# Optimization experiments

Measured on AMD Instinct MI355X. Metric: run time of the kernel, lower is better.

## Reference

```python
import jax, jax.numpy as jnp
import numpy as np

GRID_INTERVAL = 0.3  # grid_interval init arg (used as module-level global in the original source)
EPS = 1e-12
B, G, M, N_ORB, DIM = 16, 4096, 128, 400, 768


def setup_inputs() -> dict:
    key = jax.random.key(0)
    k1, k2, k3, k4, k5 = jax.random.split(key, 5)
    # distances are physical (positive); avoid d=0 so negative powers in the laplace GTO stay finite
    distance_matrices = jax.random.uniform(k1, (B, G, M), jnp.float32, 0.5, 8.0)
    quantum_numbers = jax.random.randint(k2, (B, M), 0, 3).astype(jnp.int32) + 1  # principal q in {1,2,3}
    atomic_orbitals = jax.random.randint(k3, (B, M), 0, N_ORB)
    N_electrons = jax.random.uniform(k4, (B,), jnp.float32, 2.0, 68.0)
    coefficient_table = jax.random.normal(k5, (N_ORB, DIM), jnp.float32)  # nn.Embedding(N_orbitals, dim)
    zeta_table = jnp.ones((N_ORB, 1), jnp.float32)  # nn.Embedding(N_orbitals, 1), init ones
    return dict(distance_matrices=distance_matrices,
                quantum_numbers=quantum_numbers,
                atomic_orbitals=atomic_orbitals,
                N_electrons=N_electrons,
                coefficient_table=coefficient_table,
                zeta_table=zeta_table)


def _gto_bases(d, q, z):
    """GTO and laplace-GTO basis matrices, normalized over the grid axis.
    d: [B,G,M] distances; q: [B,1,M] principal quantum numbers (float); z: [B,1,M] zetas.
    Block-diagonal pad value 1e6 in the original makes off-block entries exactly 0,
    so the per-molecule batched norm over axis=1 matches the block-diagonal column norm.
    """
    e = jnp.exp(-(z ** 2) * d ** 2)
    gto = d ** (q - 1.0) * e  # d^(q-1) * exp(-z^2 d^2)
    denom = jnp.maximum(jnp.linalg.norm(gto, axis=1, keepdims=True), EPS) * GRID_INTERVAL ** 1.5
    l_gto = d ** (q - 3.0) * e * (4.0 * z ** 4 * d ** 4
                                  - 2.0 * z ** 2 * (2.0 * q + 1.0) * d ** 2
                                  + q * (q - 1.0))
    return gto / denom, l_gto / denom


def reference(distance_matrices, quantum_numbers, atomic_orbitals, N_electrons,
              coefficient_table, zeta_table):
    Bv, Gv, Mv = distance_matrices.shape
    D = coefficient_table.shape[1]
    q = quantum_numbers.astype(distance_matrices.dtype)[:, None, :]      # [B,1,M]
    z = zeta_table[atomic_orbitals][..., 0][:, None, :]                  # [B,1,M]
    n_gto, n_l_gto = _gto_bases(distance_matrices, q, z)                 # [B,G,M]
    # LCAO coefficients: F.normalize(coefficient(AOs), 2, 0) per molecule (norm over orbital axis M)
    c = coefficient_table[atomic_orbitals]                               # [B,M,D]
    c = c / jnp.maximum(jnp.linalg.norm(c, axis=1, keepdims=True), EPS)
    mo = jnp.einsum('bgm,bmd->bgd', n_gto, c)                            # molecular orbitals
    l_mo = jnp.einsum('bgm,bmd->bgd', n_l_gto, c)                        # laplace MOs
    # normalize MOs per molecule over the grid axis, scale by sqrt(N_el/dim); laplace MOs share denom
    denom = jnp.maximum(jnp.linalg.norm(mo, axis=1, keepdims=True), EPS)
    scale = jnp.sqrt(N_electrons / D)[:, None, None]
    mo_n = scale * mo / denom
    l_mo_n = scale * l_mo / denom
    # torch.cat over molecules along the grid axis -> [B*G, D]; stack (MOs, laplace MOs)
    return jnp.stack([mo_n.reshape(Bv * Gv, D), l_mo_n.reshape(Bv * Gv, D)])
```

## Files before the change

### kernel.cpp

```cpp
#include <hip/hip_runtime.h>
#include <hip/hip_bf16.h>
#include <math.h>

#define B_    16
#define G_    4096
#define M_    128
#define D_    768
#define GI15  0.16431676725154983f
#define EPS_  1e-12f

typedef __attribute__((ext_vector_type(8))) short short8v;
typedef __attribute__((ext_vector_type(4))) float f32x4;
typedef unsigned short ushort_t;
typedef unsigned int   uint_t;

__device__ __forceinline__ ushort_t f2bf(float f) {
    uint_t u = __float_as_uint(f);
    u += 0x7FFFu + ((u >> 16) & 1u);
    return (ushort_t)(u >> 16);
}
__device__ __forceinline__ float bf2f(ushort_t h) {
    return __uint_as_float(((uint_t)h) << 16);
}

__global__ __launch_bounds__(256) void k_gram_part(
        const float* __restrict__ dist,
        const int*   __restrict__ qn,
        const int*   __restrict__ ao,
        const float* __restrict__ zeta,
        float*       __restrict__ part) {
    __shared__ float sg[64][M_];
    __shared__ float pz2[M_], pq[M_];
    const int b = blockIdx.y, ch = blockIdx.x, tid = threadIdx.x;
    if (tid < M_) {
        pq[tid] = (float)qn[b * M_ + tid];
        float z = zeta[ao[b * M_ + tid]];
        pz2[tid] = z * z;
    }
    __syncthreads();
    {
        int m = tid & 127;
        float z2 = pz2[m], q = pq[m];
        for (int r = tid >> 7; r < 64; r += 2) {
            float d = dist[((size_t)(b * G_ + ch * 64 + r)) * M_ + m];
            float e  = __expf(-z2 * d * d);
            float p1 = (q < 1.5f) ? 1.f : ((q < 2.5f) ? d : d * d);
            sg[r][m] = p1 * e;
        }
    }
    __syncthreads();
    const int mi0 = (tid >> 4) * 8;
    const int mj0 = (tid & 15) * 8;
    float acc[8][8];
    #pragma unroll
    for (int i = 0; i < 8; ++i)
        #pragma unroll
        for (int j = 0; j < 8; ++j) acc[i][j] = 0.f;
    #pragma unroll 2
    for (int g = 0; g < 64; ++g) {
        float av[8], bv[8];
        *(float4*)&av[0] = *(const float4*)&sg[g][mi0];
        *(float4*)&av[4] = *(const float4*)&sg[g][mi0 + 4];
        *(float4*)&bv[0] = *(const float4*)&sg[g][mj0];
        *(float4*)&bv[4] = *(const float4*)&sg[g][mj0 + 4];
        #pragma unroll
        for (int i = 0; i < 8; ++i)
            #pragma unroll
            for (int j = 0; j < 8; ++j)
                acc[i][j] = fmaf(av[i], bv[j], acc[i][j]);
    }
    float* pp = part + ((size_t)(ch * B_ + b)) * (M_ * M_);
    #pragma unroll
    for (int i = 0; i < 8; ++i) {
        *(float4*)&pp[(mi0 + i) * M_ + mj0]     = make_float4(acc[i][0], acc[i][1], acc[i][2], acc[i][3]);
        *(float4*)&pp[(mi0 + i) * M_ + mj0 + 4] = make_float4(acc[i][4], acc[i][5], acc[i][6], acc[i][7]);
    }
}

__global__ void k_gram_red(const float* __restrict__ part,
                           float*       __restrict__ gram) {
    int idx = blockIdx.x * 256 + threadIdx.x;
    float s = 0.f;
    #pragma unroll 8
    for (int ch = 0; ch < 64; ++ch)
        s += part[(size_t)ch * (B_ * M_ * M_) + idx];
    gram[idx] = s;
}

__global__ __launch_bounds__(256) void k_mosq(
        const float* __restrict__ gram,
        const int*   __restrict__ ao,
        const float* __restrict__ table,
        const float* __restrict__ Nel,
        float*       __restrict__ cf) {
    __shared__ float sv[M_][64];
    __shared__ float sGq[32][M_];
    __shared__ float prg[M_];
    __shared__ float sred[4][64];
    __shared__ float srcn[64];
    const int b = blockIdx.y, d0 = blockIdx.x * 64, tid = threadIdx.x;
    const int dl = tid & 63, quad = tid >> 6;
    const float* gb = gram + (size_t)b * M_ * M_;
    if (tid < M_)
        prg[tid] = 1.f / (fmaxf(sqrtf(gb[tid * M_ + tid]), EPS_) * GI15);
    #pragma unroll 4
    for (int k = 0; k < 32; ++k) {
        int m = quad * 32 + k;
        sv[m][dl] = table[(size_t)ao[b * M_ + m] * D_ + d0 + dl];
    }
    __syncthreads();
    {
        float cs = 0.f;
        #pragma unroll 4
        for (int k = 0; k < 32; ++k) { float v = sv[quad * 32 + k][dl]; cs = fmaf(v, v, cs); }
        sred[quad][dl] = cs;
    }
    __syncthreads();
    if (quad == 0)
        srcn[dl] = 1.f / fmaxf(sqrtf(sred[0][dl] + sred[1][dl] + sred[2][dl] + sred[3][dl]), EPS_);
    #pragma unroll 4
    for (int k = 0; k < 32; ++k) { int m = quad * 32 + k; sv[m][dl] *= prg[m]; }
    __syncthreads();
    float acc = 0.f;
    for (int qt = 0; qt < 4; ++qt) {
        for (int e = tid; e < 32 * M_; e += 256)
            sGq[e >> 7][e & 127] = gb[(qt * 32 + (e >> 7)) * M_ + (e & 127)];
        __syncthreads();
        #pragma unroll
        for (int mr8 = 0; mr8 < 8; ++mr8) {
            int mr = quad * 8 + mr8;
            float t0 = 0.f, t1 = 0.f, t2 = 0.f, t3 = 0.f;
            #pragma unroll 4
            for (int mc = 0; mc < M_; mc += 4) {
                t0 = fmaf(sGq[mr][mc],     sv[mc][dl],     t0);
                t1 = fmaf(sGq[mr][mc + 1], sv[mc + 1][dl], t1);
                t2 = fmaf(sGq[mr][mc + 2], sv[mc + 2][dl], t2);
                t3 = fmaf(sGq[mr][mc + 3], sv[mc + 3][dl], t3);
            }
            acc = fmaf(sv[qt * 32 + mr][dl], (t0 + t1) + (t2 + t3), acc);
        }
        __syncthreads();
    }
    sred[quad][dl] = acc;
    __syncthreads();
    if (quad == 0) {
        float qf  = fmaxf(sred[0][dl] + sred[1][dl] + sred[2][dl] + sred[3][dl], 0.f);
        float rcn = srcn[dl];
        float mo  = rcn * sqrtf(qf);
        cf[b * D_ + d0 + dl] =
            sqrtf(Nel[b] / (float)D_) / fmaxf(mo, EPS_) * rcn;
    }
}

__global__ __launch_bounds__(256, 3) void k_gemm(
        const float* __restrict__ dist,
        const int*   __restrict__ qn,
        const int*   __restrict__ ao,
        const float* __restrict__ zeta,
        const float* __restrict__ table,
        const float* __restrict__ gram,
        const float* __restrict__ cf,
        float*       __restrict__ out) {
    __shared__ ushort_t sA0[2048], sA1[2048], sA2[2048], sA3[2048];
    __shared__ ushort_t sBh[8192], sBl[8192];
    __shared__ float pz2[M_], pq[M_], prg_s[M_];
    __shared__ int   pm_ao[M_];
    __shared__ float scf_s[64];
    const int tid = threadIdx.x;
    const int b  = blockIdx.z;
    const int g0 = blockIdx.y * 64;
    const int d0 = blockIdx.x * 64;
    if (tid < M_) {
        pq[tid] = (float)qn[b * M_ + tid];
        int a = ao[b * M_ + tid];
        pm_ao[tid] = a;
        float z = zeta[a];
        pz2[tid] = z * z;
        prg_s[tid] = 1.f / (fmaxf(sqrtf(gram[(size_t)b * M_ * M_ + tid * (M_ + 1)]), EPS_) * GI15);
    } else if (tid < M_ + 64) {
        scf_s[tid - M_] = cf[b * D_ + d0 + (tid - M_)];
    }
    __syncthreads();

    {
        const int dl_ = tid & 63, quad = tid >> 6;
        float cfv = scf_s[dl_];
        #pragma unroll
        for (int mq = 0; mq < 4; ++mq) {
            int m0 = quad * 32 + mq * 8;
            ushort_t h[8], l[8];
            #pragma unroll
            for (int r = 0; r < 8; ++r) {
                int m = m0 + r;
                float v = table[(size_t)pm_ao[m] * D_ + d0 + dl_] * prg_s[m] * cfv;
                h[r] = f2bf(v);
                l[r] = f2bf(v - bf2f(h[r]));
            }
            int tgt = dl_ * 256 + ((m0 * 2) ^ ((dl_ & 7) << 4));
            *(uint4*)((char*)sBh + tgt) = *(const uint4*)&h[0];
            *(uint4*)((char*)sBl + tgt) = *(const uint4*)&l[0];
        }
    }
    __syncthreads();

    const int lane = tid & 63, w = tid >> 6;
    const int lrow = lane & 15, lk8 = (lane >> 4) * 8;
    f32x4 accm[4], accl[4];
    #pragma unroll
    for (int t = 0; t < 4; ++t) {
        accm[t] = (f32x4){0.f, 0.f, 0.f, 0.f};
        accl[t] = (f32x4){0.f, 0.f, 0.f, 0.f};
    }

    const int ml  = tid & 31;
    const int gof = tid >> 5;

    for (int kc = 0; kc < 4; ++kc) {
        {
            int m = kc * 32 + ml;
            float z2 = pz2[m], q = pq[m];
            float c4 = 4.f * z2 * z2;
            float c2 = 2.f * z2 * (2.f * q + 1.f);
            float c0 = q * (q - 1.f);
            #pragma unroll
            for (int pass = 0; pass < 8; ++pass) {
                int g = pass * 8 + gof;
                float d  = dist[((size_t)(b * G_ + g0 + g)) * M_ + m];
                float d2 = d * d;
                float e  = __expf(-z2 * d2);
                float p1 = (q < 1.5f) ? 1.f : ((q < 2.5f) ? d : d2);
                float gto  = p1 * e;
                float poly = fmaf(fmaf(c4, d2, -c2), d2, c0);
                float lg   = __fdividef(p1, d2) * e * poly;
                int o = g * 32 + ml;
                ushort_t gh = f2bf(gto);
                sA0[o] = gh;
                sA1[o] = f2bf(gto - bf2f(gh));
                ushort_t lh = f2bf(lg);
                sA2[o] = lh;
                sA3[o] = f2bf(lg - bf2f(lh));
            }
        }
        __syncthreads();
        {
            int oa = (w * 16 + lrow) * 32 + lk8;
            short8v agh = *(const short8v*)&sA0[oa];
            short8v agl = *(const short8v*)&sA1[oa];
            short8v alh = *(const short8v*)&sA2[oa];
            short8v all_= *(const short8v*)&sA3[oa];
            int kk2 = (kc * 32 + lk8) * 2;
            #pragma unroll
            for (int dt = 0; dt < 4; ++dt) {
                int dr = dt * 16 + lrow;
                int off = dr * 256 + (kk2 ^ ((dr & 7) << 4));
                short8v bh = *(const short8v*)((const char*)sBh + off);
                short8v bl = *(const short8v*)((const char*)sBl + off);
                accm[dt] = __builtin_amdgcn_mfma_f32_16x16x32_bf16(agh, bh, accm[dt], 0, 0, 0);
                accm[dt] = __builtin_amdgcn_mfma_f32_16x16x32_bf16(agh, bl, accm[dt], 0, 0, 0);
                accm[dt] = __builtin_amdgcn_mfma_f32_16x16x32_bf16(agl, bh, accm[dt], 0, 0, 0);
                accl[dt] = __builtin_amdgcn_mfma_f32_16x16x32_bf16(alh, bh, accl[dt], 0, 0, 0);
                accl[dt] = __builtin_amdgcn_mfma_f32_16x16x32_bf16(alh, bl, accl[dt], 0, 0, 0);
                accl[dt] = __builtin_amdgcn_mfma_f32_16x16x32_bf16(all_, bh, accl[dt], 0, 0, 0);
            }
        }
        __syncthreads();
    }

    const size_t HALF = (size_t)B_ * G_ * D_;
    const int grow = g0 + w * 16 + (lane >> 4) * 4;
    #pragma unroll
    for (int dt = 0; dt < 4; ++dt) {
        int dcol = d0 + dt * 16 + lrow;
        #pragma unroll
        for (int r = 0; r < 4; ++r) {
            size_t off = ((size_t)(b * G_) + grow + r) * D_ + dcol;
            out[off]        = accm[dt][r];
            out[HALF + off] = accl[dt][r];
        }
    }
}

extern "C" void kernel_launch(void* const* d_in, const int* in_sizes, int n_in,
                              void* d_out, int out_size, void* d_ws, size_t ws_size,
                              hipStream_t stream) {
    const float* dist  = (const float*)d_in[0];
    const int*   qn    = (const int*)  d_in[1];
    const int*   ao    = (const int*)  d_in[2];
    const float* Nel   = (const float*)d_in[3];
    const float* table = (const float*)d_in[4];
    const float* zeta  = (const float*)d_in[5];
    float* out = (float*)d_out;
    float* ws  = (float*)d_ws;

    float* gram = ws;
    float* cf   = ws + 262144;
    float* part = out;

    k_gram_part<<<dim3(64, B_), 256, 0, stream>>>(dist, qn, ao, zeta, part);
    k_gram_red<<<1024, 256, 0, stream>>>(part, gram);
    k_mosq<<<dim3(D_ / 64, B_), 256, 0, stream>>>(gram, ao, table, Nel, cf);
    k_gemm<<<dim3(D_ / 64, G_ / 64, B_), 256, 0, stream>>>(
        dist, qn, ao, zeta, table, gram, cf, out);
}
```

Before: 655.6 us.

## Precompute split-bf16 coefficient matrix once and widen GEMM tile to 128 columns

```diff
diff --git a/kernel.cpp b/kernel.cpp
--- a/kernel.cpp
+++ b/kernel.cpp
@@ -92,12 +92,13 @@
         const int*   __restrict__ ao,
         const float* __restrict__ table,
         const float* __restrict__ Nel,
-        float*       __restrict__ cf) {
+        ushort_t*    __restrict__ bhiG,
+        ushort_t*    __restrict__ bloG) {
     __shared__ float sv[M_][64];
     __shared__ float sGq[32][M_];
     __shared__ float prg[M_];
     __shared__ float sred[4][64];
-    __shared__ float srcn[64];
+    __shared__ float srcn[64], scf[64];
     const int b = blockIdx.y, d0 = blockIdx.x * 64, tid = threadIdx.x;
     const int dl = tid & 63, quad = tid >> 6;
     const float* gb = gram + (size_t)b * M_ * M_;
@@ -147,63 +148,72 @@
         float qf  = fmaxf(sred[0][dl] + sred[1][dl] + sred[2][dl] + sred[3][dl], 0.f);
         float rcn = srcn[dl];
         float mo  = rcn * sqrtf(qf);
-        cf[b * D_ + d0 + dl] =
-            sqrtf(Nel[b] / (float)D_) / fmaxf(mo, EPS_) * rcn;
-    }
-}
-
-__global__ __launch_bounds__(256, 3) void k_gemm(
+        scf[dl] = sqrtf(Nel[b] / (float)D_) / fmaxf(mo, EPS_) * rcn;
+    }
+    __syncthreads();
+    {
+        float cfv = scf[dl];
+        ushort_t* bh = bhiG + ((size_t)b * D_ + d0 + dl) * M_;
+        ushort_t* bl = bloG + ((size_t)b * D_ + d0 + dl) * M_;
+        #pragma unroll
+        for (int mq = 0; mq < 4; ++mq) {
+            int mb = quad * 32 + mq * 8;
+            ushort_t h[8], l[8];
+            #pragma unroll
+            for (int r = 0; r < 8; ++r) {
+                float v = sv[mb + r][dl] * cfv;
+                h[r] = f2bf(v);
+                l[r] = f2bf(v - bf2f(h[r]));
+            }
+            *(uint4*)&bh[mb] = *(const uint4*)&h[0];
+            *(uint4*)&bl[mb] = *(const uint4*)&l[0];
+        }
+    }
+}
+
+__global__ __launch_bounds__(512, 4) void k_gemm(
         const float* __restrict__ dist,
         const int*   __restrict__ qn,
         const int*   __restrict__ ao,
         const float* __restrict__ zeta,
-        const float* __restrict__ table,
-        const float* __restrict__ gram,
-        const float* __restrict__ cf,
+        const ushort_t* __restrict__ bhiG,
+        const ushort_t* __restrict__ bloG,
         float*       __restrict__ out) {
     __shared__ ushort_t sA0[2048], sA1[2048], sA2[2048], sA3[2048];
-    __shared__ ushort_t sBh[8192], sBl[8192];
-    __shared__ float pz2[M_], pq[M_], prg_s[M_];
-    __shared__ int   pm_ao[M_];
-    __shared__ float scf_s[64];
+    __shared__ ushort_t sBh[16384], sBl[16384];
     const int tid = threadIdx.x;
     const int b  = blockIdx.z;
     const int g0 = blockIdx.y * 64;
-    const int d0 = blockIdx.x * 64;
-    if (tid < M_) {
-        pq[tid] = (float)qn[b * M_ + tid];
-        int a = ao[b * M_ + tid];
-        pm_ao[tid] = a;
-        float z = zeta[a];
-        pz2[tid] = z * z;
-        prg_s[tid] = 1.f / (fmaxf(sqrtf(gram[(size_t)b * M_ * M_ + tid * (M_ + 1)]), EPS_) * GI15);
-    } else if (tid < M_ + 64) {
-        scf_s[tid - M_] = cf[b * D_ + d0 + (tid - M_)];
-    }
-    __syncthreads();
+    const int d0 = blockIdx.x * 128;
 
     {
-        const int dl_ = tid & 63, quad = tid >> 6;
-        float cfv = scf_s[dl_];
-        #pragma unroll
-        for (int mq = 0; mq < 4; ++mq) {
-            int m0 = quad * 32 + mq * 8;
-            ushort_t h[8], l[8];
-            #pragma unroll
-            for (int r = 0; r < 8; ++r) {
-                int m = m0 + r;
-                float v = table[(size_t)pm_ao[m] * D_ + d0 + dl_] * prg_s[m] * cfv;
-                h[r] = f2bf(v);
-                l[r] = f2bf(v - bf2f(h[r]));
-            }
-            int tgt = dl_ * 256 + ((m0 * 2) ^ ((dl_ & 7) << 4));
-            *(uint4*)((char*)sBh + tgt) = *(const uint4*)&h[0];
-            *(uint4*)((char*)sBl + tgt) = *(const uint4*)&l[0];
-        }
-    }
-    __syncthreads();
+        const uint_t* gh = (const uint_t*)(bhiG + ((size_t)b * D_ + d0) * M_);
+        const uint_t* gl = (const uint_t*)(bloG + ((size_t)b * D_ + d0) * M_);
+        #pragma unroll
+        for (int p = 0; p < 16; ++p) {
+            int j = p * 512 + tid;
+            int drow   = j >> 6;
+            int inrow4 = (j & 63) << 2;
+            int tgt = drow * 256 + (inrow4 ^ ((drow & 7) << 4));
+            *(uint_t*)((char*)sBh + tgt) = gh[j];
+            *(uint_t*)((char*)sBl + tgt) = gl[j];
+        }
+    }
+
+    const int ml  = tid & 31;
+    const int gof = tid >> 5;
+    float q4[4], z24[4];
+    #pragma unroll
+    for (int kc = 0; kc < 4; ++kc) {
+        int m = kc * 32 + ml;
+        q4[kc]  = (float)qn[b * M_ + m];
+        float z = zeta[ao[b * M_ + m]];
+        z24[kc] = z * z;
+    }
 
     const int lane = tid & 63, w = tid >> 6;
+    const int gsub  = (w & 3) * 16;
+    const int dhalf = (w >> 2) * 64;
     const int lrow = lane & 15, lk8 = (lane >> 4) * 8;
     f32x4 accm[4], accl[4];
     #pragma unroll
@@ -211,20 +221,18 @@
         accm[t] = (f32x4){0.f, 0.f, 0.f, 0.f};
         accl[t] = (f32x4){0.f, 0.f, 0.f, 0.f};
     }
-
-    const int ml  = tid & 31;
-    const int gof = tid >> 5;
+    __syncthreads();
 
     for (int kc = 0; kc < 4; ++kc) {
         {
             int m = kc * 32 + ml;
-            float z2 = pz2[m], q = pq[m];
+            float z2 = z24[kc], q = q4[kc];
             float c4 = 4.f * z2 * z2;
             float c2 = 2.f * z2 * (2.f * q + 1.f);
             float c0 = q * (q - 1.f);
             #pragma unroll
-            for (int pass = 0; pass < 8; ++pass) {
-                int g = pass * 8 + gof;
+            for (int pass = 0; pass < 4; ++pass) {
+                int g = pass * 16 + gof;
                 float d  = dist[((size_t)(b * G_ + g0 + g)) * M_ + m];
                 float d2 = d * d;
                 float e  = __expf(-z2 * d2);
@@ -243,7 +251,7 @@
         }
         __syncthreads();
         {
-            int oa = (w * 16 + lrow) * 32 + lk8;
+            int oa = (gsub + lrow) * 32 + lk8;
             short8v agh = *(const short8v*)&sA0[oa];
             short8v agl = *(const short8v*)&sA1[oa];
             short8v alh = *(const short8v*)&sA2[oa];
@@ -251,7 +259,7 @@
             int kk2 = (kc * 32 + lk8) * 2;
             #pragma unroll
             for (int dt = 0; dt < 4; ++dt) {
-                int dr = dt * 16 + lrow;
+                int dr = dhalf + dt * 16 + lrow;
                 int off = dr * 256 + (kk2 ^ ((dr & 7) << 4));
                 short8v bh = *(const short8v*)((const char*)sBh + off);
                 short8v bl = *(const short8v*)((const char*)sBl + off);
@@ -267,10 +275,10 @@
     }
 
     const size_t HALF = (size_t)B_ * G_ * D_;
-    const int grow = g0 + w * 16 + (lane >> 4) * 4;
+    const int grow = g0 + gsub + (lane >> 4) * 4;
     #pragma unroll
     for (int dt = 0; dt < 4; ++dt) {
-        int dcol = d0 + dt * 16 + lrow;
+        int dcol = d0 + dhalf + dt * 16 + lrow;
         #pragma unroll
         for (int r = 0; r < 4; ++r) {
             size_t off = ((size_t)(b * G_) + grow + r) * D_ + dcol;
@@ -292,13 +300,14 @@
     float* out = (float*)d_out;
     float* ws  = (float*)d_ws;
 
-    float* gram = ws;
-    float* cf   = ws + 262144;
-    float* part = out;
+    float*    gram = ws;
+    ushort_t* bhi  = (ushort_t*)(ws + 262144);
+    ushort_t* blo  = (ushort_t*)(ws + 262144 + 786432);
+    float*    part = out;
 
     k_gram_part<<<dim3(64, B_), 256, 0, stream>>>(dist, qn, ao, zeta, part);
     k_gram_red<<<1024, 256, 0, stream>>>(part, gram);
-    k_mosq<<<dim3(D_ / 64, B_), 256, 0, stream>>>(gram, ao, table, Nel, cf);
-    k_gemm<<<dim3(D_ / 64, G_ / 64, B_), 256, 0, stream>>>(
-        dist, qn, ao, zeta, table, gram, cf, out);
-}
+    k_mosq<<<dim3(D_ / 64, B_), 256, 0, stream>>>(gram, ao, table, Nel, bhi, blo);
+    k_gemm<<<dim3(D_ / 128, G_ / 64, B_), 512, 0, stream>>>(
+        dist, qn, ao, zeta, bhi, blo, out);
+}
```

After: 590.5 us. 1.11x faster.
